# Performance work log

Measured on AMD Instinct MI355X. Metric: run time of the kernel, lower is better.

## Reference

```python
import jax, jax.numpy as jnp
import numpy as np

B, S, QD, KD, VD, OD = 8, 2048, 768, 768, 768, 512

def setup_inputs() -> dict:
    key = jax.random.key(0)
    ks = jax.random.split(key, 14)
    s_q = 1.0 / np.sqrt(QD)
    s_k = 1.0 / np.sqrt(KD)
    s_v = 1.0 / np.sqrt(VD)
    return {
        "query": jax.random.normal(ks[0], (B, S, QD), jnp.float32),
        "key": jax.random.normal(ks[1], (B, S, KD), jnp.float32),
        "value": jax.random.normal(ks[2], (B, S, VD), jnp.float32),
        "Wqr": jax.random.normal(ks[3], (QD, OD), jnp.float32) * s_q,
        "bqr": jnp.zeros((OD,), jnp.float32),
        "Wqi": jax.random.normal(ks[4], (QD, OD), jnp.float32) * s_q,
        "bqi": jnp.zeros((OD,), jnp.float32),
        "Wkr": jax.random.normal(ks[5], (KD, OD), jnp.float32) * s_k,
        "bkr": jnp.zeros((OD,), jnp.float32),
        "Wki": jax.random.normal(ks[6], (KD, OD), jnp.float32) * s_k,
        "bki": jnp.zeros((OD,), jnp.float32),
        "Wv": jax.random.normal(ks[7], (VD, OD), jnp.float32) * s_v,
        "bv": jnp.zeros((OD,), jnp.float32),
        "coherence_weight": jnp.asarray(1.0, jnp.float32),
    }

def reference(query, key, value, Wqr, bqr, Wqi, bqi, Wkr, bkr, Wki, bki, Wv, bv, coherence_weight):
    # Complex-valued projections (real/imag parts via separate linears)
    q_r = jnp.einsum("bsq,qo->bso", query, Wqr) + bqr
    q_i = jnp.einsum("bsq,qo->bso", query, Wqi) + bqi
    k_r = jnp.einsum("bsk,ko->bso", key, Wkr) + bkr
    k_i = jnp.einsum("bsk,ko->bso", key, Wki) + bki
    v = jnp.einsum("bsv,vo->bso", value, Wv) + bv
    # Complex QK^T: (q_r + i q_i)(k_r - i k_i)^T pieces, as in the torch code
    att_real = jnp.einsum("bso,bto->bst", q_r, k_r) + jnp.einsum("bso,bto->bst", q_i, k_i)
    att_imag = jnp.einsum("bso,bto->bst", q_i, k_r) - jnp.einsum("bso,bto->bst", q_r, k_i)
    att_mag = jnp.sqrt(att_real ** 2 + att_imag ** 2)
    scale = jnp.asarray(1.0 / np.sqrt(OD), att_mag.dtype)
    weights = jax.nn.softmax(att_mag * scale, axis=-1)  # [B,S,S]
    output = jnp.einsum("bst,bto->bso", weights, v)  # [B,S,OD]
    coherence = jnp.mean(att_imag ** 2) * coherence_weight
    return output, coherence
```

## Files before the change

kernel.cpp:

```cpp
#include <hip/hip_runtime.h>
#include <math.h>
#include <stdint.h>

#define S_    2048
#define SCALE_ 0.044194173824159216f

typedef __attribute__((ext_vector_type(8))) short short8;
typedef __attribute__((ext_vector_type(4))) float f32x4;

#define MFMA16(a, b, c) __builtin_amdgcn_mfma_f32_16x16x32_bf16((a), (b), (c), 0, 0, 0)

__device__ __forceinline__ void glds16(const void* g, void* l) {
  __builtin_amdgcn_global_load_lds(
      (const __attribute__((address_space(1))) void*)g,
      (__attribute__((address_space(3))) void*)l, 16, 0, 0);
}

__device__ __forceinline__ unsigned short f2bf(float f) {
  unsigned u = __float_as_uint(f);
  u += 0x7FFFu + ((u >> 16) & 1u);
  return (unsigned short)(u >> 16);
}

__global__ __launch_bounds__(256) void convert3_kernel(
    const float* __restrict__ a, const float* __restrict__ b,
    const float* __restrict__ c, unsigned short* __restrict__ oa,
    unsigned short* __restrict__ ob, unsigned short* __restrict__ oc) {
  int i = blockIdx.x * 256 + threadIdx.x;
  int which = i / 3145728;
  int off = i - which * 3145728;
  const float* s = (which == 0) ? a : (which == 1) ? b : c;
  unsigned short* d = (which == 0) ? oa : (which == 1) ? ob : oc;
  float4 v = ((const float4*)s)[off];
  ushort4 o;
  o.x = f2bf(v.x); o.y = f2bf(v.y); o.z = f2bf(v.z); o.w = f2bf(v.w);
  ((ushort4*)d)[off] = o;
}

__global__ void bias_build_kernel(const float* bqr, const float* bqi,
                                  const float* bkr, const float* bki,
                                  const float* bv, float* bq, float* bk,
                                  float* bvo) {
  int t = blockIdx.x * 256 + threadIdx.x;
  if (t < 512) { bq[t] = bqr[t]; bk[t] = bkr[t]; bvo[t] = bv[t]; }
  else if (t < 1024) { bq[t] = bqi[t - 512]; bk[t] = bki[t - 512]; }
}

__global__ __launch_bounds__(256) void wtrans_kernel(
    const float* __restrict__ W, unsigned short* __restrict__ Wt, int N,
    int row_off) {
  __shared__ float t[32][33];
  int n0 = blockIdx.x * 32, k0 = blockIdx.y * 32;
  int tx = threadIdx.x & 31, ty = threadIdx.x >> 5;
#pragma unroll
  for (int r = 0; r < 4; ++r)
    t[ty + r * 8][tx] = W[(size_t)(k0 + ty + r * 8) * N + n0 + tx];
  __syncthreads();
#pragma unroll
  for (int r = 0; r < 4; ++r)
    Wt[(size_t)(row_off + n0 + ty + r * 8) * 768 + k0 + tx] =
        f2bf(t[tx][ty + r * 8]);
}

__global__ void init_kernel(float* lsum, float* coh) {
  int t = blockIdx.x * 256 + threadIdx.x;
  if (t < 16384) lsum[t] = 0.f;
  if (t == 0) *coh = 0.f;
}

__global__ __launch_bounds__(256, 2) void proj_kernel(
    const unsigned short* __restrict__ Xb, const unsigned short* __restrict__ Wt,
    const float* __restrict__ bias, unsigned short* __restrict__ Y, int N,
    int vt_mode) {
  __shared__ char lds[65536];
  const int tid = threadIdx.x;
  const int lane = tid & 63, wid = tid >> 6;
  const int wi = wid >> 1, wj = wid & 1;
  const int m0 = blockIdx.y * 128, n0 = blockIdx.x * 128;
  const char* Xc = (const char*)Xb;
  const char* Wc = (const char*)Wt;
  const int tile = wid >> 1;

  const char* sp[8];
  int sd[8];
#pragma unroll
  for (int iss = 0; iss < 8; ++iss) {
    int gbase = wid * 512 + iss * 64;
    int loc = (gbase & 1023) + lane;
    int r = loc >> 3, blk = loc & 7;
    int sb = blk ^ (r & 7);
    sp[iss] = (tile == 0) ? Xc + (size_t)(m0 + r) * 1536 + sb * 16
                          : Wc + (size_t)(n0 + r) * 1536 + sb * 16;
    sd[iss] = gbase * 16;
  }

  f32x4 acc[4][4] = {};

#pragma unroll
  for (int iss = 0; iss < 8; ++iss) glds16(sp[iss], lds + sd[iss]);

  for (int s = 0; s < 12; ++s) {
    __syncthreads();
    if (s + 1 < 12) {
      char* wb = lds + ((s + 1) & 1) * 32768;
#pragma unroll
      for (int iss = 0; iss < 8; ++iss)
        glds16(sp[iss] + (s + 1) * 128, wb + sd[iss]);
    }
    const char* rb = lds + (s & 1) * 32768;
#pragma unroll
    for (int kk = 0; kk < 2; ++kk) {
      int blk = kk * 4 + (lane >> 4);
      short8 a[4];
#pragma unroll
      for (int i = 0; i < 4; ++i) {
        int row = wi * 64 + i * 16 + (lane & 15);
        a[i] = *(const short8*)(rb + row * 128 + ((blk ^ (row & 7)) << 4));
      }
#pragma unroll
      for (int j = 0; j < 4; ++j) {
        int row = wj * 64 + j * 16 + (lane & 15);
        short8 b = *(const short8*)(rb + 16384 + row * 128 +
                                    ((blk ^ (row & 7)) << 4));
#pragma unroll
        for (int i = 0; i < 4; ++i) acc[i][j] = MFMA16(a[i], b, acc[i][j]);
      }
    }
  }

#pragma unroll
  for (int j = 0; j < 4; ++j) {
    int n = n0 + wj * 64 + j * 16 + (lane & 15);
    float bn = bias[n];
    if (!vt_mode) {
#pragma unroll
      for (int i = 0; i < 4; ++i) {
        int mrow = m0 + wi * 64 + i * 16 + (lane >> 4) * 4;
#pragma unroll
        for (int r = 0; r < 4; ++r)
          Y[(size_t)(mrow + r) * N + n] = f2bf(acc[i][j][r] + bn);
      }
    } else {
#pragma unroll
      for (int i = 0; i < 4; ++i) {
        int mrow = m0 + wi * 64 + i * 16 + (lane >> 4) * 4;
        int b = mrow >> 11, key = mrow & 2047;
        ushort4 o;
        o.x = f2bf(acc[i][j][0] + bn);
        o.y = f2bf(acc[i][j][1] + bn);
        o.z = f2bf(acc[i][j][2] + bn);
        o.w = f2bf(acc[i][j][3] + bn);
        *(ushort4*)&Y[((size_t)b * 512 + n) * 2048 + key] = o;
      }
    }
  }
}

__global__ __launch_bounds__(256, 2) void score_kernel(
    const unsigned short* __restrict__ Qcat,
    const unsigned short* __restrict__ Kcat, unsigned short* __restrict__ P,
    float* __restrict__ lsum, float* __restrict__ coh) {
  __shared__ char lds[65536];
  const int tid = threadIdx.x;
  const int lane = tid & 63, wid = tid >> 6;
  const int wm = wid >> 1;
  const int wn = wid & 1;
  const int lr = lane & 15;
  const int lk = lane >> 4;
  const int l8 = lane >> 3, lb = lane & 7;

  const int id = blockIdx.x;
  const int w = (id & 7) * 256 + (id >> 3);
  const int batch = w >> 8;
  const int tilein = w & 255;
  const int q0 = (tilein >> 4) << 7;
  const int k0 = (tilein & 15) << 7;

  const char* Qc = (const char*)Qcat + ((size_t)batch * 2048 + q0) * 2048;
  const char* Kc = (const char*)Kcat + ((size_t)batch * 2048 + k0) * 2048;

  const char* sp[8];
  int sd[8];
#pragma unroll
  for (int u = 0; u < 8; ++u) {
    int L = wid * 8 + u;
    int row = ((L & 15) << 3) + l8;
    int sb = lb ^ (row & 7);
    const char* base = (L < 16) ? Qc : Kc;
    sp[u] = base + (size_t)row * 2048 + (sb & 3) * 16 + (sb >> 2) * 1024;
    sd[u] = L << 10;
  }

  int aoff_lo[4], aoff_hi[4], boff_lo[4], boff_hi[4];
#pragma unroll
  for (int i = 0; i < 4; ++i) {
    int ar = wm * 64 + i * 16 + lr;
    aoff_lo[i] = ar * 128 + ((lk ^ (ar & 7)) << 4);
    aoff_hi[i] = ar * 128 + (((4 + lk) ^ (ar & 7)) << 4);
  }
#pragma unroll
  for (int j = 0; j < 4; ++j) {
    int br = wn * 64 + j * 16 + lr;
    boff_lo[j] = 16384 + br * 128 + ((lk ^ (br & 7)) << 4);
    boff_hi[j] = 16384 + br * 128 + (((4 + lk) ^ (br & 7)) << 4);
  }

  f32x4 accre[4][4] = {}, accim[4][4] = {};
  const short sg = (short)0x8000;
  const short8 SGN = {sg, sg, sg, sg, sg, sg, sg, sg};

#pragma unroll
  for (int u = 0; u < 8; ++u) glds16(sp[u], lds + sd[u]);

  for (int t = 0; t < 16; ++t) {
    __syncthreads();
    if (t + 1 < 16) {
      char* wb = lds + ((t + 1) & 1) * 32768;
#pragma unroll
      for (int u = 0; u < 8; ++u)
        glds16(sp[u] + (t + 1) * 64, wb + sd[u]);
    }
    const char* rb = lds + (t & 1) * 32768;
    short8 alo[4], ahi[4];
#pragma unroll
    for (int i = 0; i < 4; ++i) {
      alo[i] = *(const short8*)(rb + aoff_lo[i]);
      ahi[i] = *(const short8*)(rb + aoff_hi[i]);
    }
#pragma unroll
    for (int j = 0; j < 4; ++j) {
      short8 blo = *(const short8*)(rb + boff_lo[j]);
      short8 bhi = *(const short8*)(rb + boff_hi[j]);
      short8 bhin = bhi ^ SGN;
#pragma unroll
      for (int i = 0; i < 4; ++i) {
        accre[i][j] = MFMA16(alo[i], blo, accre[i][j]);
        accre[i][j] = MFMA16(ahi[i], bhi, accre[i][j]);
        accim[i][j] = MFMA16(ahi[i], blo, accim[i][j]);
        accim[i][j] = MFMA16(alo[i], bhin, accim[i][j]);
      }
    }
  }

  float csum = 0.f;
  size_t prow_base = (size_t)batch * 2048;
#pragma unroll
  for (int i = 0; i < 4; ++i) {
#pragma unroll
    for (int r = 0; r < 4; ++r) {
      int row = q0 + wm * 64 + i * 16 + lk * 4 + r;
      unsigned short* prow = P + (prow_base + row) * 2048;
      float rs = 0.f;
#pragma unroll
      for (int j = 0; j < 4; ++j) {
        float re = accre[i][j][r], im = accim[i][j][r];
        csum += im * im;
        float p = __expf(sqrtf(re * re + im * im) * SCALE_);
        rs += p;
        prow[k0 + wn * 64 + j * 16 + lr] = f2bf(p);
      }
      rs += __shfl_xor(rs, 1, 64);
      rs += __shfl_xor(rs, 2, 64);
      rs += __shfl_xor(rs, 4, 64);
      rs += __shfl_xor(rs, 8, 64);
      if (lr == 0) atomicAdd(&lsum[prow_base + row], rs);
    }
  }
#pragma unroll
  for (int m = 1; m < 64; m <<= 1) csum += __shfl_xor(csum, m, 64);
  float* cred = (float*)lds;
  __syncthreads();
  if (lane == 0) cred[wid] = csum;
  __syncthreads();
  if (tid == 0) atomicAdd(coh, cred[0] + cred[1] + cred[2] + cred[3]);
}

__global__ __launch_bounds__(256, 2) void pv_kernel(
    const unsigned short* __restrict__ P, const unsigned short* __restrict__ Vt,
    const float* __restrict__ lsum, float* __restrict__ out) {
  __shared__ char lds[65536];
  const int tid = threadIdx.x;
  const int lane = tid & 63, wid = tid >> 6;
  const int wi = wid >> 1, wj = wid & 1;

  int id = blockIdx.x;
  int w = (id & 7) * 64 + (id >> 3);
  int batch = w >> 6, tilein = w & 63;
  int i0 = (tilein >> 2) * 128;
  int o0 = (tilein & 3) * 128;

  const char* Pc = (const char*)P + (size_t)batch * 2048 * 4096;
  const char* Vc = (const char*)Vt + (size_t)batch * 512 * 4096;
  const int tile = wid >> 1;

  const char* sp[8];
  int sd[8];
#pragma unroll
  for (int iss = 0; iss < 8; ++iss) {
    int gbase = wid * 512 + iss * 64;
    int loc = (gbase & 1023) + lane;
    int r = loc >> 3, blk = loc & 7;
    int sb = blk ^ (r & 7);
    sp[iss] = (tile == 0) ? Pc + (size_t)(i0 + r) * 4096 + sb * 16
                          : Vc + (size_t)(o0 + r) * 4096 + sb * 16;
    sd[iss] = gbase * 16;
  }

  f32x4 acc[4][4] = {};

#pragma unroll
  for (int iss = 0; iss < 8; ++iss) glds16(sp[iss], lds + sd[iss]);

  for (int s = 0; s < 32; ++s) {
    __syncthreads();
    if (s + 1 < 32) {
      char* wb = lds + ((s + 1) & 1) * 32768;
#pragma unroll
      for (int iss = 0; iss < 8; ++iss)
        glds16(sp[iss] + (s + 1) * 128, wb + sd[iss]);
    }
    const char* rb = lds + (s & 1) * 32768;
#pragma unroll
    for (int kk = 0; kk < 2; ++kk) {
      int blk = kk * 4 + (lane >> 4);
      short8 a[4];
#pragma unroll
      for (int i = 0; i < 4; ++i) {
        int row = wi * 64 + i * 16 + (lane & 15);
        a[i] = *(const short8*)(rb + row * 128 + ((blk ^ (row & 7)) << 4));
      }
#pragma unroll
      for (int j = 0; j < 4; ++j) {
        int row = wj * 64 + j * 16 + (lane & 15);
        short8 b = *(const short8*)(rb + 16384 + row * 128 +
                                    ((blk ^ (row & 7)) << 4));
#pragma unroll
        for (int i = 0; i < 4; ++i) acc[i][j] = MFMA16(a[i], b, acc[i][j]);
      }
    }
  }

#pragma unroll
  for (int i = 0; i < 4; ++i) {
    int mrow = i0 + wi * 64 + i * 16 + (lane >> 4) * 4;
    float linv[4];
#pragma unroll
    for (int r = 0; r < 4; ++r)
      linv[r] = 1.0f / lsum[(size_t)batch * 2048 + mrow + r];
#pragma unroll
    for (int j = 0; j < 4; ++j) {
      int n = o0 + wj * 64 + j * 16 + (lane & 15);
#pragma unroll
      for (int r = 0; r < 4; ++r)
        out[((size_t)batch * 2048 + mrow + r) * 512 + n] = acc[i][j][r] * linv[r];
    }
  }
}

__global__ void finalize_kernel(const float* __restrict__ coh,
                                const float* __restrict__ cw,
                                float* __restrict__ out_last) {
  *out_last = (*coh) * (1.0f / 33554432.0f) * (*cw);
}

extern "C" void kernel_launch(void* const* d_in, const int* in_sizes, int n_in,
                              void* d_out, int out_size, void* d_ws,
                              size_t ws_size, hipStream_t stream) {
  const float* query = (const float*)d_in[0];
  const float* key   = (const float*)d_in[1];
  const float* value = (const float*)d_in[2];
  const float* Wqr = (const float*)d_in[3];
  const float* bqr = (const float*)d_in[4];
  const float* Wqi = (const float*)d_in[5];
  const float* bqi = (const float*)d_in[6];
  const float* Wkr = (const float*)d_in[7];
  const float* bkr = (const float*)d_in[8];
  const float* Wki = (const float*)d_in[9];
  const float* bki = (const float*)d_in[10];
  const float* Wv  = (const float*)d_in[11];
  const float* bv  = (const float*)d_in[12];
  const float* cw  = (const float*)d_in[13];
  float* out = (float*)d_out;

  char* ws = (char*)d_ws;
  unsigned short* XQ   = (unsigned short*)(ws + 0);
  unsigned short* XK   = (unsigned short*)(ws + 25165824);
  unsigned short* XV   = (unsigned short*)(ws + 50331648);
  unsigned short* Pbuf = (unsigned short*)(ws + 0);
  unsigned short* WTQ  = (unsigned short*)(ws + 75497472);
  unsigned short* WTK  = (unsigned short*)(ws + 77070336);
  unsigned short* WTV  = (unsigned short*)(ws + 78643200);
  float* BQ   = (float*)(ws + 79429632);
  float* BK   = (float*)(ws + 79433728);
  float* BV   = (float*)(ws + 79437824);
  unsigned short* QCAT = (unsigned short*)(ws + 79441920);
  unsigned short* KCAT = (unsigned short*)(ws + 112996352);
  unsigned short* VT   = (unsigned short*)(ws + 146550784);
  float* LSUM = (float*)(ws + 163328000);
  float* COH  = (float*)(ws + 163393536);
  if (ws_size < 163393600) return;

  convert3_kernel<<<36864, 256, 0, stream>>>(query, key, value, XQ, XK, XV);
  bias_build_kernel<<<4, 256, 0, stream>>>(bqr, bqi, bkr, bki, bv, BQ, BK, BV);
  wtrans_kernel<<<dim3(16, 24), 256, 0, stream>>>(Wqr, WTQ, 512, 0);
  wtrans_kernel<<<dim3(16, 24), 256, 0, stream>>>(Wqi, WTQ, 512, 512);
  wtrans_kernel<<<dim3(16, 24), 256, 0, stream>>>(Wkr, WTK, 512, 0);
  wtrans_kernel<<<dim3(16, 24), 256, 0, stream>>>(Wki, WTK, 512, 512);
  wtrans_kernel<<<dim3(16, 24), 256, 0, stream>>>(Wv, WTV, 512, 0);

  proj_kernel<<<dim3(8, 128), 256, 0, stream>>>(XQ, WTQ, BQ, QCAT, 1024, 0);
  proj_kernel<<<dim3(8, 128), 256, 0, stream>>>(XK, WTK, BK, KCAT, 1024, 0);
  proj_kernel<<<dim3(4, 128), 256, 0, stream>>>(XV, WTV, BV, VT, 512, 1);

  init_kernel<<<64, 256, 0, stream>>>(LSUM, COH);
  score_kernel<<<2048, 256, 0, stream>>>(QCAT, KCAT, Pbuf, LSUM, COH);
  pv_kernel<<<512, 256, 0, stream>>>(Pbuf, VT, LSUM, out);
  finalize_kernel<<<1, 1, 0, stream>>>(COH, cw, out + 8388608);
}
```

Measured before the change: 346.8 us.

## Fuse fp32-to-bf16 input conversion into projection GEMM and stage score stores via LDS

Removes the separate convert kernel: the projection kernel now loads fp32 activations directly, converts them to bf16 in registers, and writes the swizzled tiles to LDS, while weights still arrive via global_load_lds. The score kernel writes its bf16 probabilities to a padded LDS tile first and then emits coalesced 16-byte row stores instead of scattered 2-byte global stores. Small setup kernels (bias, init, five weight transposes) are merged into two launches. This avoids the bf16 copy's write-and-reread traffic, but the A operand now loads synchronously through registers and loses the async LDS path.

New measurement: 374.1 us. +7.9%, slower.

```diff
diff --git a/kernel.cpp b/kernel.cpp
--- a/kernel.cpp
+++ b/kernel.cpp
@@ -22,39 +22,41 @@
   return (unsigned short)(u >> 16);
 }
 
-__global__ __launch_bounds__(256) void convert3_kernel(
-    const float* __restrict__ a, const float* __restrict__ b,
-    const float* __restrict__ c, unsigned short* __restrict__ oa,
-    unsigned short* __restrict__ ob, unsigned short* __restrict__ oc) {
-  int i = blockIdx.x * 256 + threadIdx.x;
-  int which = i / 3145728;
-  int off = i - which * 3145728;
-  const float* s = (which == 0) ? a : (which == 1) ? b : c;
-  unsigned short* d = (which == 0) ? oa : (which == 1) ? ob : oc;
-  float4 v = ((const float4*)s)[off];
-  ushort4 o;
-  o.x = f2bf(v.x); o.y = f2bf(v.y); o.z = f2bf(v.z); o.w = f2bf(v.w);
-  ((ushort4*)d)[off] = o;
-}
-
-__global__ void bias_build_kernel(const float* bqr, const float* bqi,
-                                  const float* bkr, const float* bki,
-                                  const float* bv, float* bq, float* bk,
-                                  float* bvo) {
+__global__ void init_fused_kernel(const float* __restrict__ bqr,
+                                  const float* __restrict__ bqi,
+                                  const float* __restrict__ bkr,
+                                  const float* __restrict__ bki,
+                                  const float* __restrict__ bv, float* bq,
+                                  float* bk, float* bvo, float* lsum,
+                                  float* coh) {
   int t = blockIdx.x * 256 + threadIdx.x;
   if (t < 512) { bq[t] = bqr[t]; bk[t] = bkr[t]; bvo[t] = bv[t]; }
   else if (t < 1024) { bq[t] = bqi[t - 512]; bk[t] = bki[t - 512]; }
-}
-
-__global__ __launch_bounds__(256) void wtrans_kernel(
-    const float* __restrict__ W, unsigned short* __restrict__ Wt, int N,
-    int row_off) {
+  if (t < 16384) lsum[t] = 0.f;
+  if (t == 0) *coh = 0.f;
+}
+
+__global__ __launch_bounds__(256) void wtrans_all_kernel(
+    const float* __restrict__ Wqr, const float* __restrict__ Wqi,
+    const float* __restrict__ Wkr, const float* __restrict__ Wki,
+    const float* __restrict__ Wv, unsigned short* __restrict__ WTQ,
+    unsigned short* __restrict__ WTK, unsigned short* __restrict__ WTV) {
   __shared__ float t[32][33];
+  const float* W;
+  unsigned short* Wt;
+  int row_off;
+  switch (blockIdx.z) {
+    case 0: W = Wqr; Wt = WTQ; row_off = 0; break;
+    case 1: W = Wqi; Wt = WTQ; row_off = 512; break;
+    case 2: W = Wkr; Wt = WTK; row_off = 0; break;
+    case 3: W = Wki; Wt = WTK; row_off = 512; break;
+    default: W = Wv; Wt = WTV; row_off = 0; break;
+  }
   int n0 = blockIdx.x * 32, k0 = blockIdx.y * 32;
   int tx = threadIdx.x & 31, ty = threadIdx.x >> 5;
 #pragma unroll
   for (int r = 0; r < 4; ++r)
-    t[ty + r * 8][tx] = W[(size_t)(k0 + ty + r * 8) * N + n0 + tx];
+    t[ty + r * 8][tx] = W[(size_t)(k0 + ty + r * 8) * 512 + n0 + tx];
   __syncthreads();
 #pragma unroll
   for (int r = 0; r < 4; ++r)
@@ -62,14 +64,8 @@
         f2bf(t[tx][ty + r * 8]);
 }
 
-__global__ void init_kernel(float* lsum, float* coh) {
-  int t = blockIdx.x * 256 + threadIdx.x;
-  if (t < 16384) lsum[t] = 0.f;
-  if (t == 0) *coh = 0.f;
-}
-
 __global__ __launch_bounds__(256, 2) void proj_kernel(
-    const unsigned short* __restrict__ Xb, const unsigned short* __restrict__ Wt,
+    const float* __restrict__ X, const unsigned short* __restrict__ Wt,
     const float* __restrict__ bias, unsigned short* __restrict__ Y, int N,
     int vt_mode) {
   __shared__ char lds[65536];
@@ -77,35 +73,53 @@
   const int lane = tid & 63, wid = tid >> 6;
   const int wi = wid >> 1, wj = wid & 1;
   const int m0 = blockIdx.y * 128, n0 = blockIdx.x * 128;
-  const char* Xc = (const char*)Xb;
   const char* Wc = (const char*)Wt;
-  const int tile = wid >> 1;
-
-  const char* sp[8];
-  int sd[8];
-#pragma unroll
-  for (int iss = 0; iss < 8; ++iss) {
-    int gbase = wid * 512 + iss * 64;
-    int loc = (gbase & 1023) + lane;
+
+  const int c4 = tid & 15, r0 = tid >> 4;
+  const float* xrow[8];
+  int adst[8];
+#pragma unroll
+  for (int rep = 0; rep < 8; ++rep) {
+    int row = r0 + rep * 16;
+    xrow[rep] = X + (size_t)(m0 + row) * 768 + c4 * 4;
+    adst[rep] = row * 128 + (((c4 >> 1) ^ (row & 7)) << 4) + (c4 & 1) * 8;
+  }
+  const char* bsp[4];
+  int bsd[4];
+#pragma unroll
+  for (int iss = 0; iss < 4; ++iss) {
+    int loc = (wid * 4 + iss) * 64 + lane;
     int r = loc >> 3, blk = loc & 7;
     int sb = blk ^ (r & 7);
-    sp[iss] = (tile == 0) ? Xc + (size_t)(m0 + r) * 1536 + sb * 16
-                          : Wc + (size_t)(n0 + r) * 1536 + sb * 16;
-    sd[iss] = gbase * 16;
+    bsp[iss] = Wc + (size_t)(n0 + r) * 1536 + sb * 16;
+    bsd[iss] = 16384 + (wid * 4 + iss) * 1024;
   }
 
   f32x4 acc[4][4] = {};
 
-#pragma unroll
-  for (int iss = 0; iss < 8; ++iss) glds16(sp[iss], lds + sd[iss]);
+  auto stageB = [&](char* wb, int s) {
+#pragma unroll
+    for (int iss = 0; iss < 4; ++iss) glds16(bsp[iss] + s * 128, wb + bsd[iss]);
+  };
+  auto stageA = [&](char* wb, int s) {
+#pragma unroll
+    for (int rep = 0; rep < 8; ++rep) {
+      float4 v = *(const float4*)(xrow[rep] + s * 64);
+      ushort4 o;
+      o.x = f2bf(v.x); o.y = f2bf(v.y); o.z = f2bf(v.z); o.w = f2bf(v.w);
+      *(ushort4*)(wb + adst[rep]) = o;
+    }
+  };
+
+  stageB(lds, 0);
+  stageA(lds, 0);
 
   for (int s = 0; s < 12; ++s) {
     __syncthreads();
     if (s + 1 < 12) {
       char* wb = lds + ((s + 1) & 1) * 32768;
-#pragma unroll
-      for (int iss = 0; iss < 8; ++iss)
-        glds16(sp[iss] + (s + 1) * 128, wb + sd[iss]);
+      stageB(wb, s + 1);
+      stageA(wb, s + 1);
     }
     const char* rb = lds + (s & 1) * 32768;
 #pragma unroll
@@ -217,8 +231,7 @@
     if (t + 1 < 16) {
       char* wb = lds + ((t + 1) & 1) * 32768;
 #pragma unroll
-      for (int u = 0; u < 8; ++u)
-        glds16(sp[u] + (t + 1) * 64, wb + sd[u]);
+      for (int u = 0; u < 8; ++u) glds16(sp[u] + (t + 1) * 64, wb + sd[u]);
     }
     const char* rb = lds + (t & 1) * 32768;
     short8 alo[4], ahi[4];
@@ -242,14 +255,15 @@
     }
   }
 
+  __syncthreads();
+  char* pt = lds;
   float csum = 0.f;
   size_t prow_base = (size_t)batch * 2048;
 #pragma unroll
   for (int i = 0; i < 4; ++i) {
 #pragma unroll
     for (int r = 0; r < 4; ++r) {
-      int row = q0 + wm * 64 + i * 16 + lk * 4 + r;
-      unsigned short* prow = P + (prow_base + row) * 2048;
+      int row16 = wm * 64 + i * 16 + lk * 4 + r;
       float rs = 0.f;
 #pragma unroll
       for (int j = 0; j < 4; ++j) {
@@ -257,19 +271,29 @@
         csum += im * im;
         float p = __expf(sqrtf(re * re + im * im) * SCALE_);
         rs += p;
-        prow[k0 + wn * 64 + j * 16 + lr] = f2bf(p);
+        *(unsigned short*)(pt + row16 * 272 + (wn * 64 + j * 16 + lr) * 2) =
+            f2bf(p);
       }
       rs += __shfl_xor(rs, 1, 64);
       rs += __shfl_xor(rs, 2, 64);
       rs += __shfl_xor(rs, 4, 64);
       rs += __shfl_xor(rs, 8, 64);
-      if (lr == 0) atomicAdd(&lsum[prow_base + row], rs);
+      if (lr == 0) atomicAdd(&lsum[prow_base + q0 + row16], rs);
     }
   }
 #pragma unroll
   for (int m = 1; m < 64; m <<= 1) csum += __shfl_xor(csum, m, 64);
-  float* cred = (float*)lds;
   __syncthreads();
+  {
+    const int c16 = tid & 15, rr0 = tid >> 4;
+#pragma unroll
+    for (int rep = 0; rep < 8; ++rep) {
+      int row = rr0 + rep * 16;
+      short8 v = *(const short8*)(pt + row * 272 + c16 * 16);
+      *(short8*)&P[(prow_base + q0 + row) * 2048 + k0 + c16 * 8] = v;
+    }
+  }
+  float* cred = (float*)(lds + 36864);
   if (lane == 0) cred[wid] = csum;
   __syncthreads();
   if (tid == 0) atomicAdd(coh, cred[0] + cred[1] + cred[2] + cred[3]);
@@ -383,9 +407,6 @@
   float* out = (float*)d_out;
 
   char* ws = (char*)d_ws;
-  unsigned short* XQ   = (unsigned short*)(ws + 0);
-  unsigned short* XK   = (unsigned short*)(ws + 25165824);
-  unsigned short* XV   = (unsigned short*)(ws + 50331648);
   unsigned short* Pbuf = (unsigned short*)(ws + 0);
   unsigned short* WTQ  = (unsigned short*)(ws + 75497472);
   unsigned short* WTK  = (unsigned short*)(ws + 77070336);
@@ -400,19 +421,15 @@
   float* COH  = (float*)(ws + 163393536);
   if (ws_size < 163393600) return;
 
-  convert3_kernel<<<36864, 256, 0, stream>>>(query, key, value, XQ, XK, XV);
-  bias_build_kernel<<<4, 256, 0, stream>>>(bqr, bqi, bkr, bki, bv, BQ, BK, BV);
-  wtrans_kernel<<<dim3(16, 24), 256, 0, stream>>>(Wqr, WTQ, 512, 0);
-  wtrans_kernel<<<dim3(16, 24), 256, 0, stream>>>(Wqi, WTQ, 512, 512);
-  wtrans_kernel<<<dim3(16, 24), 256, 0, stream>>>(Wkr, WTK, 512, 0);
-  wtrans_kernel<<<dim3(16, 24), 256, 0, stream>>>(Wki, WTK, 512, 512);
-  wtrans_kernel<<<dim3(16, 24), 256, 0, stream>>>(Wv, WTV, 512, 0);
-
-  proj_kernel<<<dim3(8, 128), 256, 0, stream>>>(XQ, WTQ, BQ, QCAT, 1024, 0);
-  proj_kernel<<<dim3(8, 128), 256, 0, stream>>>(XK, WTK, BK, KCAT, 1024, 0);
-  proj_kernel<<<dim3(4, 128), 256, 0, stream>>>(XV, WTV, BV, VT, 512, 1);
-
-  init_kernel<<<64, 256, 0, stream>>>(LSUM, COH);
+  init_fused_kernel<<<64, 256, 0, stream>>>(bqr, bqi, bkr, bki, bv, BQ, BK, BV,
+                                            LSUM, COH);
+  wtrans_all_kernel<<<dim3(16, 24, 5), 256, 0, stream>>>(Wqr, Wqi, Wkr, Wki, Wv,
+                                                         WTQ, WTK, WTV);
+
+  proj_kernel<<<dim3(8, 128), 256, 0, stream>>>(query, WTQ, BQ, QCAT, 1024, 0);
+  proj_kernel<<<dim3(8, 128), 256, 0, stream>>>(key, WTK, BK, KCAT, 1024, 0);
+  proj_kernel<<<dim3(4, 128), 256, 0, stream>>>(value, WTV, BV, VT, 512, 1);
+
   score_kernel<<<2048, 256, 0, stream>>>(QCAT, KCAT, Pbuf, LSUM, COH);
   pv_kernel<<<512, 256, 0, stream>>>(Pbuf, VT, LSUM, out);
   finalize_kernel<<<1, 1, 0, stream>>>(COH, cw, out + 8388608);
```
